# Kernel tuning notes

Hardware: AMD Instinct MI355X
Metric: run time of the kernel (lower is better)

The kernel has to match this reference:

```python
import jax, jax.numpy as jnp
import numpy as np

C = 1.0          # ball curvature magnitude (manifold.c)
EPS = 1e-5       # boundary projection epsilon
MIN_NORM = 1e-15

def _norm(x):
    return jnp.maximum(jnp.linalg.norm(x, axis=-1, keepdims=True), MIN_NORM)

def artanh(x):
    return jnp.arctanh(jnp.clip(x, -1.0 + 1e-7, 1.0 - 1e-7))

def proj(x, c=C):
    # clip points to the open Poincare ball of radius 1/sqrt(c)
    n = _norm(x)
    maxnorm = (1.0 - EPS) / jnp.sqrt(c)
    return jnp.where(n > maxnorm, x / n * maxnorm, x)

def logmap0(x, c=C):
    sc = jnp.sqrt(c)
    n = _norm(x)
    return artanh(sc * n) * x / (sc * n)

def expmap0(u, c=C):
    sc = jnp.sqrt(c)
    n = _norm(u)
    return jnp.tanh(sc * n) * u / (sc * n)

def gyro_add(x, y, c=C):
    # Mobius (gyrovector) addition
    x2 = jnp.sum(x * x, -1, keepdims=True)
    y2 = jnp.sum(y * y, -1, keepdims=True)
    xy = jnp.sum(x * y, -1, keepdims=True)
    num = (1.0 + 2.0 * c * xy + c * y2) * x + (1.0 - c * x2) * y
    den = 1.0 + 2.0 * c * xy + c * c * x2 * y2
    return num / jnp.maximum(den, MIN_NORM)

def gyro_matvec(W, x, c=C):
    # Mobius matrix-vector multiplication (pv_gyro_matvec)
    sc = jnp.sqrt(c)
    xn = _norm(x)
    mx = x @ W.T                       # [N, out]
    mxn = _norm(mx)
    res = jnp.tanh(mxn / xn * artanh(sc * xn)) * mx / (mxn * sc)
    zero = jnp.all(mx == 0.0, axis=-1, keepdims=True)
    return jnp.where(zero, jnp.zeros_like(res), res)

def hyp_linear(x, W, b, c=C):
    # CustomHyperbolicLinear (activation=None branch): mobius matvec + hyp bias gyro-add
    res = proj(gyro_matvec(W, x, c), c)
    hyp_bias = proj(expmap0(b[None, :], c), c)   # proj_tan0 is identity on the ball
    res = proj(gyro_add(res, hyp_bias, c), c)
    return res

def hyp_tanh_act(x, c=C):
    # CustomHyperbolicActivation(manifold, nn.Tanh()): tanh in tangent space at origin
    x = proj(x, c)
    t = jnp.tanh(logmap0(x, c))
    return proj(expmap0(t, c), c)


def setup_inputs() -> dict:
    key = jax.random.key(0)
    k0, k1, k2 = jax.random.split(key, 3)
    N, D, H = 32768, 1024, 1024
    x = proj(0.1 * jax.random.normal(k0, (N, D), dtype=jnp.float32))
    gain = float(np.sqrt(2.0))
    bound1 = gain * float(np.sqrt(6.0 / (D + H)))   # xavier_uniform with gain sqrt(2)
    W1 = jax.random.uniform(k1, (H, D), jnp.float32, -bound1, bound1)
    b1 = jnp.zeros((H,), jnp.float32)
    bound2 = gain * float(np.sqrt(6.0 / (H + H)))
    W2 = jax.random.uniform(k2, (H, H), jnp.float32, -bound2, bound2)
    b2 = jnp.zeros((H,), jnp.float32)
    return {"x": x, "W1": W1, "b1": b1, "W2": W2, "b2": b2}


def reference(x, W1, b1, W2, b2):
    # GeometricModel forward: two CustomHyperbolicLayer blocks
    # (hyperbolic linear -> tangent-space tanh activation)
    h = hyp_linear(x, W1, b1)
    h = hyp_tanh_act(h)
    h = hyp_linear(h, W2, b2)
    h = hyp_tanh_act(h)
    return h
```

## Files before the change

kernel.cpp:

```cpp
#include <hip/hip_runtime.h>


typedef short short8 __attribute__((ext_vector_type(8)));
typedef unsigned short u16x8 __attribute__((ext_vector_type(8)));
typedef unsigned short u16x4 __attribute__((ext_vector_type(4)));
typedef float f32x4 __attribute__((ext_vector_type(4)));

#define MAXN (1.0f - 1e-5f)

__device__ __forceinline__ float bf2f(unsigned short u) {
    return __uint_as_float(((unsigned int)u) << 16);
}
__device__ __forceinline__ unsigned short f2bf(float f) {
    unsigned int u = __float_as_uint(f);
    u += 0x7FFFu + ((u >> 16) & 1u);
    return (unsigned short)(u >> 16);
}
__device__ __forceinline__ float wave_sum(float v) {
#pragma unroll
    for (int m = 32; m > 0; m >>= 1) v += __shfl_xor(v, m, 64);
    return v;
}
__device__ __forceinline__ float artanh_clip(float x) {
    x = fminf(fmaxf(x, -1.0f + 1e-7f), 1.0f - 1e-7f);
    return 0.5f * logf((1.0f + x) / (1.0f - x));
}

__device__ __forceinline__ void gld_lds16(const unsigned short* g, unsigned short* l) {
    __builtin_amdgcn_global_load_lds(
        (const __attribute__((address_space(1))) unsigned int*)g,
        (__attribute__((address_space(3))) unsigned int*)l,
        16, 0, 0);
}

__global__ __launch_bounds__(256) void cast_x_kernel(
    const float* __restrict__ X, unsigned short* __restrict__ Xb,
    float* __restrict__ xn, int K)
{
    int row = blockIdx.x * 4 + (threadIdx.x >> 6);
    int l = threadIdx.x & 63;
    const float4* xr = (const float4*)(X + (size_t)row * K);
    u16x4* xw = (u16x4*)(Xb + (size_t)row * K);
    float ss = 0.f;
#pragma unroll
    for (int i = 0; i < 4; ++i) {
        float4 v = xr[i * 64 + l];
        ss += v.x * v.x + v.y * v.y + v.z * v.z + v.w * v.w;
        u16x4 o;
        o[0] = f2bf(v.x); o[1] = f2bf(v.y); o[2] = f2bf(v.z); o[3] = f2bf(v.w);
        xw[i * 64 + l] = o;
    }
    ss = wave_sum(ss);
    if (l == 0) xn[row] = fmaxf(sqrtf(ss), 1e-15f);
}

__global__ __launch_bounds__(256) void cast_w_kernel(
    const float* __restrict__ W, unsigned short* __restrict__ Wb, int n4)
{
    int i = blockIdx.x * 256 + threadIdx.x;
    if (i >= n4) return;
    float4 v = ((const float4*)W)[i];
    u16x4 o;
    o[0] = f2bf(v.x); o[1] = f2bf(v.y); o[2] = f2bf(v.z); o[3] = f2bf(v.w);
    ((u16x4*)Wb)[i] = o;
}

__global__ __launch_bounds__(256) void gemm_bt_kernel(
    const unsigned short* __restrict__ A,
    const unsigned short* __restrict__ B,
    unsigned short* __restrict__ C,
    int M, int Nc, int K)
{
    __shared__ __align__(16) unsigned short sA[128 * 32];
    __shared__ __align__(16) unsigned short sB[128 * 32];

    const int t = threadIdx.x;
    const int l = t & 63;
    const int w = t >> 6;
    const int nb = Nc >> 7;
    const int bm = blockIdx.x / nb;
    const int bn = blockIdx.x % nb;

    const unsigned short* Ab = A + (size_t)bm * 128 * K;
    const unsigned short* Bb = B + (size_t)bn * 128 * K;

    const int wm = (w >> 1) * 64;
    const int wn = (w & 1) * 64;
    const int lr = l & 15;
    const int lq = l >> 4;

    const int idx0 = t, idx1 = t + 256;
    const size_t ga0 = (size_t)(idx0 >> 2) * K + (idx0 & 3) * 8;
    const size_t ga1 = (size_t)(idx1 >> 2) * K + (idx1 & 3) * 8;

    f32x4 acc[4][4];
#pragma unroll
    for (int i = 0; i < 4; ++i)
#pragma unroll
        for (int j = 0; j < 4; ++j)
            acc[i][j] = (f32x4){0.f, 0.f, 0.f, 0.f};

    for (int kt = 0; kt < K; kt += 32) {
        __syncthreads();
        gld_lds16(Ab + ga0 + kt, &sA[idx0 * 8]);
        gld_lds16(Ab + ga1 + kt, &sA[idx1 * 8]);
        gld_lds16(Bb + ga0 + kt, &sB[idx0 * 8]);
        gld_lds16(Bb + ga1 + kt, &sB[idx1 * 8]);
        __syncthreads();

        short8 av[4], bv[4];
#pragma unroll
        for (int i = 0; i < 4; ++i)
            av[i] = *(const short8*)&sA[(wm + i * 16 + lr) * 32 + lq * 8];
#pragma unroll
        for (int j = 0; j < 4; ++j)
            bv[j] = *(const short8*)&sB[(wn + j * 16 + lr) * 32 + lq * 8];
#pragma unroll
        for (int i = 0; i < 4; ++i)
#pragma unroll
            for (int j = 0; j < 4; ++j)
                acc[i][j] = __builtin_amdgcn_mfma_f32_16x16x32_bf16(av[i], bv[j], acc[i][j], 0, 0, 0);
    }

    unsigned short* Cb = C + (size_t)(bm * 128 + wm) * Nc + bn * 128 + wn;
#pragma unroll
    for (int i = 0; i < 4; ++i)
#pragma unroll
        for (int j = 0; j < 4; ++j)
#pragma unroll
            for (int r = 0; r < 4; ++r)
                Cb[(size_t)(i * 16 + lq * 4 + r) * Nc + j * 16 + lr] = f2bf(acc[i][j][r]);
}

template <int OUTF32>
__global__ __launch_bounds__(256) void hyp_epilogue_kernel(
    const unsigned short* __restrict__ mx, const float* __restrict__ xn_in,
    const float* __restrict__ bvec, void* __restrict__ outp,
    float* __restrict__ xn_out, int H)
{
    int row = blockIdx.x * 4 + (threadIdx.x >> 6);
    int l = threadIdx.x & 63;
    const u16x8* mrow = (const u16x8*)(mx + (size_t)row * H);
    u16x8 mv0 = mrow[l], mv1 = mrow[64 + l];
    const float4* bf4 = (const float4*)bvec;
    float4 bq0 = bf4[l * 2], bq1 = bf4[l * 2 + 1];
    float4 bq2 = bf4[128 + l * 2], bq3 = bf4[128 + l * 2 + 1];

    float m[16], b[16];
#pragma unroll
    for (int i = 0; i < 8; ++i) { m[i] = bf2f(mv0[i]); m[8 + i] = bf2f(mv1[i]); }
    b[0] = bq0.x; b[1] = bq0.y; b[2] = bq0.z; b[3] = bq0.w;
    b[4] = bq1.x; b[5] = bq1.y; b[6] = bq1.z; b[7] = bq1.w;
    b[8] = bq2.x; b[9] = bq2.y; b[10] = bq2.z; b[11] = bq2.w;
    b[12] = bq3.x; b[13] = bq3.y; b[14] = bq3.z; b[15] = bq3.w;

    float ssm = 0.f, ssb = 0.f, dmb = 0.f;
#pragma unroll
    for (int i = 0; i < 16; ++i) {
        ssm += m[i] * m[i]; ssb += b[i] * b[i]; dmb += m[i] * b[i];
    }
    ssm = wave_sum(ssm); ssb = wave_sum(ssb); dmb = wave_sum(dmb);

    float mxn = fmaxf(sqrtf(ssm), 1e-15f);
    float bn  = fmaxf(sqrtf(ssb), 1e-15f);
    float xn  = xn_in[row];

    float tt = tanhf(mxn / xn * artanh_clip(xn));
    float rnorm = fabsf(tt);
    float pr = (rnorm > MAXN) ? (MAXN / rnorm) : 1.0f;
    float resScale = tt * pr / mxn;
    float rn = fminf(rnorm, MAXN);
    float x2 = rn * rn;

    float tb = tanhf(bn);
    float hbn = fabsf(tb);
    float pb = (hbn > MAXN) ? (MAXN / hbn) : 1.0f;
    float hscale = (tb / bn) * pb;
    float hn = fminf(hbn, MAXN);
    float y2 = hn * hn;

    float xy = resScale * hscale * dmb;
    float ca = 1.0f + 2.0f * xy + y2;
    float cb = 1.0f - x2;
    float den = fmaxf(1.0f + 2.0f * xy + x2 * y2, 1e-15f);
    float fA = ca * resScale / den;
    float fB = cb * hscale / den;

    float ssz = fA * fA * ssm + 2.0f * fA * fB * dmb + fB * fB * ssb;
    float zn = fmaxf(sqrtf(fmaxf(ssz, 0.0f)), 1e-15f);
    float pz = (zn > MAXN) ? (MAXN / zn) : 1.0f;
    float n2 = fmaxf(fminf(zn, MAXN), 1e-15f);
    float g = (artanh_clip(n2) / n2) * pz;

    float u[16];
    float ssu = 0.f;
#pragma unroll
    for (int i = 0; i < 16; ++i) {
        float zi = fA * m[i] + fB * b[i];
        u[i] = tanhf(g * zi);
        ssu += u[i] * u[i];
    }
    ssu = wave_sum(ssu);
    float un = fmaxf(sqrtf(ssu), 1e-15f);
    float te = tanhf(un);
    float on = fabsf(te);
    float po = (on > MAXN) ? (MAXN / on) : 1.0f;
    float os = (te / un) * po;

    if (OUTF32) {
        float* of = (float*)outp + (size_t)row * H;
        float4* of4 = (float4*)of;
        float4 a0, a1, a2, a3;
        a0.x = os * u[0];  a0.y = os * u[1];  a0.z = os * u[2];  a0.w = os * u[3];
        a1.x = os * u[4];  a1.y = os * u[5];  a1.z = os * u[6];  a1.w = os * u[7];
        a2.x = os * u[8];  a2.y = os * u[9];  a2.z = os * u[10]; a2.w = os * u[11];
        a3.x = os * u[12]; a3.y = os * u[13]; a3.z = os * u[14]; a3.w = os * u[15];
        of4[l * 2] = a0; of4[l * 2 + 1] = a1;
        of4[128 + l * 2] = a2; of4[128 + l * 2 + 1] = a3;
    } else {
        u16x8 o0, o1;
#pragma unroll
        for (int i = 0; i < 8; ++i) { o0[i] = f2bf(os * u[i]); o1[i] = f2bf(os * u[8 + i]); }
        u16x8* orow = (u16x8*)((unsigned short*)outp + (size_t)row * H);
        orow[l] = o0; orow[64 + l] = o1;
    }
    if (l == 0) xn_out[row] = fmaxf(fminf(on, MAXN), 1e-15f);
}

extern "C" void kernel_launch(void* const* d_in, const int* in_sizes, int n_in,
                              void* d_out, int out_size, void* d_ws, size_t ws_size,
                              hipStream_t stream)
{
    const float* x  = (const float*)d_in[0];
    const float* W1 = (const float*)d_in[1];
    const float* b1 = (const float*)d_in[2];
    const float* W2 = (const float*)d_in[3];
    const float* b2 = (const float*)d_in[4];

    const int H = in_sizes[2];
    const int D = in_sizes[1] / H;
    const int N = in_sizes[0] / D;

    unsigned short* stage = (unsigned short*)d_out;
    float* outf = (float*)d_out;

    unsigned short* mxb = (unsigned short*)d_ws;
    unsigned short* W1b = mxb + (size_t)N * H;
    unsigned short* W2b = W1b + (size_t)H * D;
    float* xn1 = (float*)(W2b + (size_t)H * H);
    float* xn2 = xn1 + N;

    dim3 blk(256);
    const int gemm_grid = (N / 128) * (H / 128);

    cast_x_kernel<<<N / 4, blk, 0, stream>>>(x, stage, xn1, D);
    cast_w_kernel<<<(H * D / 4 + 255) / 256, blk, 0, stream>>>(W1, W1b, H * D / 4);
    cast_w_kernel<<<(H * H / 4 + 255) / 256, blk, 0, stream>>>(W2, W2b, H * H / 4);
    gemm_bt_kernel<<<gemm_grid, blk, 0, stream>>>(stage, W1b, mxb, N, H, D);
    hyp_epilogue_kernel<0><<<N / 4, blk, 0, stream>>>(mxb, xn1, b1, stage, xn2, H);
    gemm_bt_kernel<<<gemm_grid, blk, 0, stream>>>(stage, W2b, mxb, N, H, H);
    hyp_epilogue_kernel<1><<<N / 4, blk, 0, stream>>>(mxb, xn2, b2, outf, xn1, H);
}
```

Baseline: 521.1 us.

## Rework bf16 GEMM into 256x256 tiles with 4-stage LDS pipeline and swizzle

The GEMM moves from 128x128 tiles with a single LDS buffer to 256x256 tiles run by 512 threads. Global-to-LDS loads are prefetched through a 4-deep ring, with explicit vmcnt waits and one barrier per k-step. An XOR swizzle on the LDS layout targets bank conflicts, and a blockIdx remap targets L2 locality. This should hide memory latency and raise MFMA reuse per loaded byte, but it uses 128KB of LDS per block and more accumulator registers, which may limit occupancy.

```diff
diff --git a/kernel.cpp b/kernel.cpp
--- a/kernel.cpp
+++ b/kernel.cpp
@@ -65,71 +65,107 @@
     ((u16x4*)Wb)[i] = o;
 }
 
-__global__ __launch_bounds__(256) void gemm_bt_kernel(
+#define STAGE(rs_, kt_) do {                                            \
+    const int ko_ = (kt_) << 5;                                         \
+    gld_lds16(Ab + ga0 + ko_, &sA[(rs_) * 8192 + c0 * 8]);              \
+    gld_lds16(Ab + ga1 + ko_, &sA[(rs_) * 8192 + c1 * 8]);              \
+    gld_lds16(Bb + ga0 + ko_, &sB[(rs_) * 8192 + c0 * 8]);              \
+    gld_lds16(Bb + ga1 + ko_, &sB[(rs_) * 8192 + c1 * 8]);              \
+} while (0)
+
+#define KSTEP(kt_, DOSTAGE_, VMSTR_, DOSYNC_) {                                     \
+    if (DOSTAGE_) { STAGE(((kt_) + 3) & 3, (kt_) + 3); }                            \
+    const int rb_ = ((kt_) & 3) * 8192;                                             \
+    const unsigned short* pa_ = &sA[rb_ + (wm + lr) * 32 + swo];                    \
+    const unsigned short* pb_ = &sB[rb_ + (wn + lr) * 32 + swo];                    \
+    short8 av_[8]; short8 bv_[4];                                                   \
+    _Pragma("unroll")                                                               \
+    for (int m_ = 0; m_ < 8; ++m_) av_[m_] = *(const short8*)(pa_ + m_ * 512);      \
+    _Pragma("unroll")                                                               \
+    for (int n_ = 0; n_ < 4; ++n_) bv_[n_] = *(const short8*)(pb_ + n_ * 512);      \
+    __builtin_amdgcn_s_setprio(1);                                                  \
+    _Pragma("unroll")                                                               \
+    for (int m_ = 0; m_ < 8; ++m_)                                                  \
+        _Pragma("unroll")                                                           \
+        for (int n_ = 0; n_ < 4; ++n_)                                              \
+            acc[m_][n_] = __builtin_amdgcn_mfma_f32_16x16x32_bf16(                  \
+                av_[m_], bv_[n_], acc[m_][n_], 0, 0, 0);                            \
+    __builtin_amdgcn_s_setprio(0);                                                  \
+    if (DOSYNC_) {                                                                  \
+        asm volatile("s_waitcnt vmcnt(" VMSTR_ ")" ::: "memory");                   \
+        __builtin_amdgcn_s_barrier();                                               \
+    }                                                                               \
+}
+
+__global__ __launch_bounds__(512, 2) void gemm_bt_kernel(
     const unsigned short* __restrict__ A,
     const unsigned short* __restrict__ B,
     unsigned short* __restrict__ C,
     int M, int Nc, int K)
 {
-    __shared__ __align__(16) unsigned short sA[128 * 32];
-    __shared__ __align__(16) unsigned short sB[128 * 32];
+    __shared__ __align__(16) unsigned short sA[4 * 256 * 32];
+    __shared__ __align__(16) unsigned short sB[4 * 256 * 32];
 
     const int t = threadIdx.x;
     const int l = t & 63;
     const int w = t >> 6;
-    const int nb = Nc >> 7;
-    const int bm = blockIdx.x / nb;
-    const int bn = blockIdx.x % nb;
-
-    const unsigned short* Ab = A + (size_t)bm * 128 * K;
-    const unsigned short* Bb = B + (size_t)bn * 128 * K;
-
-    const int wm = (w >> 1) * 64;
-    const int wn = (w & 1) * 64;
     const int lr = l & 15;
     const int lq = l >> 4;
 
-    const int idx0 = t, idx1 = t + 256;
-    const size_t ga0 = (size_t)(idx0 >> 2) * K + (idx0 & 3) * 8;
-    const size_t ga1 = (size_t)(idx1 >> 2) * K + (idx1 & 3) * 8;
-
-    f32x4 acc[4][4];
-#pragma unroll
-    for (int i = 0; i < 4; ++i)
+    const int nwg = gridDim.x;
+    const int cpx = nwg >> 3;
+    const int swz = (blockIdx.x & 7) * cpx + (blockIdx.x >> 3);
+    const int nb = Nc >> 8;
+    const int bm = swz / nb;
+    const int bn = swz % nb;
+
+    const unsigned short* Ab = A + (size_t)bm * 256 * K;
+    const unsigned short* Bb = B + (size_t)bn * 256 * K;
+
+    const int wm = (w >> 2) * 128;
+    const int wn = (w & 3) * 64;
+
+    const int c0 = t, c1 = t + 512;
+    const int r0 = c0 >> 2, s0 = (c0 & 3) ^ ((r0 >> 1) & 3);
+    const int r1 = c1 >> 2, s1 = (c1 & 3) ^ ((r1 >> 1) & 3);
+    const size_t ga0 = (size_t)r0 * K + s0 * 8;
+    const size_t ga1 = (size_t)r1 * K + s1 * 8;
+
+    const int swo = (lq ^ ((lr >> 1) & 3)) * 8;
+
+    f32x4 acc[8][4];
+#pragma unroll
+    for (int i = 0; i < 8; ++i)
 #pragma unroll
         for (int j = 0; j < 4; ++j)
             acc[i][j] = (f32x4){0.f, 0.f, 0.f, 0.f};
 
-    for (int kt = 0; kt < K; kt += 32) {
-        __syncthreads();
-        gld_lds16(Ab + ga0 + kt, &sA[idx0 * 8]);
-        gld_lds16(Ab + ga1 + kt, &sA[idx1 * 8]);
-        gld_lds16(Bb + ga0 + kt, &sB[idx0 * 8]);
-        gld_lds16(Bb + ga1 + kt, &sB[idx1 * 8]);
-        __syncthreads();
-
-        short8 av[4], bv[4];
-#pragma unroll
-        for (int i = 0; i < 4; ++i)
-            av[i] = *(const short8*)&sA[(wm + i * 16 + lr) * 32 + lq * 8];
-#pragma unroll
-        for (int j = 0; j < 4; ++j)
-            bv[j] = *(const short8*)&sB[(wn + j * 16 + lr) * 32 + lq * 8];
-#pragma unroll
-        for (int i = 0; i < 4; ++i)
+    STAGE(0, 0);
+    STAGE(1, 1);
+    STAGE(2, 2);
+    asm volatile("s_waitcnt vmcnt(8)" ::: "memory");
+    __builtin_amdgcn_s_barrier();
+
+    const int NTK = K >> 5;
+    int kt = 0;
+#pragma unroll 1
+    for (; kt < NTK - 3; ++kt) {
+        KSTEP(kt, true, "8", true);
+    }
+    KSTEP(kt, false, "4", true); ++kt;
+    KSTEP(kt, false, "0", true); ++kt;
+    KSTEP(kt, false, "0", false);
+
+    unsigned short* Cb = C + (size_t)(bm * 256 + wm) * Nc + bn * 256 + wn;
+#pragma unroll
+    for (int i = 0; i < 8; ++i)
+#pragma unroll
+        for (int r = 0; r < 4; ++r) {
+            unsigned short* Cr = Cb + (size_t)(i * 16 + lq * 4 + r) * Nc + lr;
 #pragma unroll
             for (int j = 0; j < 4; ++j)
-                acc[i][j] = __builtin_amdgcn_mfma_f32_16x16x32_bf16(av[i], bv[j], acc[i][j], 0, 0, 0);
-    }
-
-    unsigned short* Cb = C + (size_t)(bm * 128 + wm) * Nc + bn * 128 + wn;
-#pragma unroll
-    for (int i = 0; i < 4; ++i)
-#pragma unroll
-        for (int j = 0; j < 4; ++j)
-#pragma unroll
-            for (int r = 0; r < 4; ++r)
-                Cb[(size_t)(i * 16 + lq * 4 + r) * Nc + j * 16 + lr] = f2bf(acc[i][j][r]);
+                Cr[j * 16] = f2bf(acc[i][j][r]);
+        }
 }
 
 template <int OUTF32>
@@ -251,13 +287,14 @@
     float* xn2 = xn1 + N;
 
     dim3 blk(256);
-    const int gemm_grid = (N / 128) * (H / 128);
+    dim3 gblk(512);
+    const int gemm_grid = (N / 256) * (H / 256);
 
     cast_x_kernel<<<N / 4, blk, 0, stream>>>(x, stage, xn1, D);
     cast_w_kernel<<<(H * D / 4 + 255) / 256, blk, 0, stream>>>(W1, W1b, H * D / 4);
     cast_w_kernel<<<(H * H / 4 + 255) / 256, blk, 0, stream>>>(W2, W2b, H * H / 4);
-    gemm_bt_kernel<<<gemm_grid, blk, 0, stream>>>(stage, W1b, mxb, N, H, D);
+    gemm_bt_kernel<<<gemm_grid, gblk, 0, stream>>>(stage, W1b, mxb, N, H, D);
     hyp_epilogue_kernel<0><<<N / 4, blk, 0, stream>>>(mxb, xn1, b1, stage, xn2, H);
-    gemm_bt_kernel<<<gemm_grid, blk, 0, stream>>>(stage, W2b, mxb, N, H, H);
+    gemm_bt_kernel<<<gemm_grid, gblk, 0, stream>>>(stage, W2b, mxb, N, H, H);
     hyp_epilogue_kernel<1><<<N / 4, blk, 0, stream>>>(mxb, xn2, b2, outf, xn1, H);
 }
```

Measured after the change: 468.8 us. 1.11x faster.
